# Optimization experiments

Hardware: AMD Instinct MI355X
Metric: run time of the kernel (lower is better)

## Reference

```python
import jax, jax.numpy as jnp
import numpy as np

SIGMA = 2048.0
N, D = 8192, 1024


def setup_inputs() -> dict:
    key = jax.random.key(0)
    kx, ky = jax.random.split(key)
    x = jax.random.normal(kx, (N, D), dtype=jnp.float32)
    y = jax.random.normal(ky, (N, D), dtype=jnp.float32)
    return {"x": x, "y": y}


def reference(x, y):
    x = x.astype(jnp.float32)
    y = y.astype(jnp.float32)
    # squared L2 norms, shape (N, 1)
    xn = jnp.sum(x * x, axis=1, keepdims=True)
    yn = jnp.sum(y * y, axis=1, keepdims=True)
    # Gram matrices (N, N)
    xx = x @ x.T
    xy = x @ y.T
    yy = y @ y.T
    first = jnp.mean(jnp.exp(-(xn + xn.T - 2.0 * xx) / SIGMA))
    second = jnp.mean(jnp.exp(-(yn + yn.T - 2.0 * yy) / SIGMA))
    third = jnp.mean(jnp.exp(-(xn + yn.T - 2.0 * xy) / SIGMA))
    return first + second - 2.0 * third
```

## Files before the change

kernel.cpp:

```cpp
#include <hip/hip_runtime.h>
#include <hip/hip_bf16.h>


#define N_ROWS 8192
#define DIM 1024
#define TWO_N 16384
#define BT 256
#define BK 64
#define NT2 64
#define NBLK2 (NT2 * (NT2 + 1) / 2)
#define GRID2 2048
#define NKT (DIM / BK)
#define QSCL (127.0f / 6.0f)
#define S2 ((6.0f / 127.0f) * (6.0f / 127.0f))
#define KFAC (-S2 / 2048.0f)

typedef int i32x4 __attribute__((ext_vector_type(4)));

typedef __attribute__((address_space(3))) unsigned int lds_u32_t;
typedef const __attribute__((address_space(1))) unsigned int glb_u32_t;

__device__ __forceinline__ void gload16(const void* g, void* l) {
    __builtin_amdgcn_global_load_lds((glb_u32_t*)g, (lds_u32_t*)l, 16, 0, 0);
}

#define SBAR() do { __builtin_amdgcn_sched_barrier(0); \
                    __builtin_amdgcn_s_barrier();      \
                    __builtin_amdgcn_sched_barrier(0); } while (0)
#define VMCNT(n) asm volatile("s_waitcnt vmcnt(" #n ")" ::: "memory")

__global__ __launch_bounds__(256) void mmd_convert_i8(const float* __restrict__ x,
                                                      const float* __restrict__ y,
                                                      int* __restrict__ zq,
                                                      int* __restrict__ zn) {
    int row = blockIdx.x * 4 + (threadIdx.x >> 6);
    int lane = threadIdx.x & 63;
    const float* p = (row < N_ROWS) ? (x + (size_t)row * DIM)
                                    : (y + (size_t)(row - N_ROWS) * DIM);
    int* q = zq + (size_t)row * (DIM / 4);
    int s = 0;
#pragma unroll
    for (int c = 0; c < 4; ++c) {
        int widx = lane + c * 64;
        float4 v = *(const float4*)(p + widx * 4);
        int q0 = (int)rintf(fminf(fmaxf(v.x * QSCL, -127.0f), 127.0f));
        int q1 = (int)rintf(fminf(fmaxf(v.y * QSCL, -127.0f), 127.0f));
        int q2 = (int)rintf(fminf(fmaxf(v.z * QSCL, -127.0f), 127.0f));
        int q3 = (int)rintf(fminf(fmaxf(v.w * QSCL, -127.0f), 127.0f));
        s += q0 * q0 + q1 * q1 + q2 * q2 + q3 * q3;
        q[widx] = (q0 & 0xff) | ((q1 & 0xff) << 8) | ((q2 & 0xff) << 16) | ((q3 & 0xff) << 24);
    }
#pragma unroll
    for (int o = 32; o > 0; o >>= 1) s += __shfl_down(s, o);
    if (lane == 0) zn[row] = s;
}

__global__ __launch_bounds__(512, 2) void mmd_main_i8(const char* __restrict__ zq,
                                                      const int* __restrict__ zn,
                                                      double* __restrict__ partials) {
    __shared__ __align__(16) char lsA[2][BT * BK];
    __shared__ __align__(16) char lsB[2][BT * BK];
    __shared__ double red[8];

    const int tid = threadIdx.x;
    const int bid0 = blockIdx.x;

    const int l = tid & 63;
    const int wid = tid >> 6;
    const int wr = wid >> 2;
    const int wc = wid & 3;
    const int fr = l & 15;
    const int fg = l >> 4;

    const int srow = tid >> 2;
    const int cswz = ((tid & 3) ^ ((tid >> 3) & 3)) * 16;
    char* lA = &lsA[0][0];
    char* lB = &lsB[0][0];
    const int t16 = tid * 16;

#define STG_A(buf, half, kt) \
    gload16(pA + (size_t)((half) * 128) * DIM + (kt) * BK, lA + (buf) * 16384 + (half) * 8192 + t16)
#define STG_B(buf, half, kt) \
    gload16(pB + (size_t)((half) * 128) * DIM + (kt) * BK, lB + (buf) * 16384 + (half) * 8192 + t16)
#define DS_A(buf, m) (*(const i32x4*)(lA + (buf) * 16384 + \
        (wr * 128 + (m) * 16 + fr) * 64 + ((fg ^ (((wr * 128 + (m) * 16 + fr) >> 1) & 3)) << 4)))
#define DS_B(buf, n) (*(const i32x4*)(lB + (buf) * 16384 + \
        (wc * 64 + (n) * 16 + fr) * 64 + ((fg ^ (((wc * 64 + (n) * 16 + fr) >> 1) & 3)) << 4)))

    const int npairs = (bid0 < NBLK2 - GRID2) ? 2 : 1;

#pragma unroll 1
    for (int pp = 0; pp < npairs; ++pp) {
        const int pid = pp ? (GRID2 + bid0) : bid0;
        const int bid = (pid & 7) * (NBLK2 / 8) + (pid >> 3);

        int tj = (int)((sqrtf(8.0f * (float)bid + 1.0f) - 1.0f) * 0.5f);
        while ((tj + 1) * (tj + 2) / 2 <= bid) ++tj;
        while (tj * (tj + 1) / 2 > bid) --tj;
        const int ti = bid - tj * (tj + 1) / 2;

        const int rA = ti * BT, rB = tj * BT;
        const float w = ((ti < 32) == (tj < 32)) ? 1.0f : -1.0f;
        const float factor = (ti == tj) ? w : 2.0f * w;

        const char* pA = zq + (size_t)(rA + srow) * DIM + cswz;
        const char* pB = zq + (size_t)(rB + srow) * DIM + cswz;

        i32x4 acc[8][4];
#pragma unroll
        for (int m = 0; m < 8; ++m)
#pragma unroll
            for (int n = 0; n < 4; ++n) acc[m][n] = (i32x4){0, 0, 0, 0};

        STG_A(0, 0, 0);
        STG_B(0, 0, 0);
        STG_B(0, 1, 0);
        STG_A(0, 1, 0);
        STG_A(1, 0, 1);
        VMCNT(1);
        SBAR();

        i32x4 a[4], b_cur[2], b_hi[2], b_nxt[2];
#pragma unroll
        for (int j = 0; j < 2; ++j) b_cur[j] = DS_B(0, j);

        for (int C = 0; C < NKT; ++C) {
            const int cb = C & 1, nb = cb ^ 1;

#pragma unroll
            for (int i = 0; i < 4; ++i) a[i] = DS_A(cb, i);
#pragma unroll
            for (int j = 0; j < 2; ++j) b_hi[j] = DS_B(cb, 2 + j);
            if (C < NKT - 1) STG_B(nb, 0, C + 1);
            SBAR();
            __builtin_amdgcn_s_setprio(1);
#pragma unroll
            for (int i = 0; i < 4; ++i)
#pragma unroll
                for (int j = 0; j < 2; ++j)
                    acc[i][j] = __builtin_amdgcn_mfma_i32_16x16x64_i8(a[i], b_cur[j], acc[i][j], 0, 0, 0);
            __builtin_amdgcn_s_setprio(0);
            SBAR();

            if (C < NKT - 1) STG_B(nb, 1, C + 1);
            SBAR();
            __builtin_amdgcn_s_setprio(1);
#pragma unroll
            for (int i = 0; i < 4; ++i)
#pragma unroll
                for (int j = 0; j < 2; ++j)
                    acc[i][2 + j] = __builtin_amdgcn_mfma_i32_16x16x64_i8(a[i], b_hi[j], acc[i][2 + j], 0, 0, 0);
            __builtin_amdgcn_s_setprio(0);
            SBAR();

#pragma unroll
            for (int i = 0; i < 4; ++i) a[i] = DS_A(cb, 4 + i);
            if (C < NKT - 1) {
                STG_A(nb, 1, C + 1);
                VMCNT(1);
            }
            SBAR();
            __builtin_amdgcn_s_setprio(1);
#pragma unroll
            for (int i = 0; i < 4; ++i)
#pragma unroll
                for (int j = 0; j < 2; ++j)
                    acc[4 + i][j] = __builtin_amdgcn_mfma_i32_16x16x64_i8(a[i], b_cur[j], acc[4 + i][j], 0, 0, 0);
            __builtin_amdgcn_s_setprio(0);
            SBAR();

            if (C < NKT - 1) {
#pragma unroll
                for (int j = 0; j < 2; ++j) b_nxt[j] = DS_B(nb, j);
                if (C < NKT - 2) {
                    STG_A(cb, 0, C + 2);
                    VMCNT(1);
                } else {
                    VMCNT(0);
                }
            }
            SBAR();
            __builtin_amdgcn_s_setprio(1);
#pragma unroll
            for (int i = 0; i < 4; ++i)
#pragma unroll
                for (int j = 0; j < 2; ++j)
                    acc[4 + i][2 + j] = __builtin_amdgcn_mfma_i32_16x16x64_i8(a[i], b_hi[j], acc[4 + i][2 + j], 0, 0, 0);
            __builtin_amdgcn_s_setprio(0);
            SBAR();

            if (C < NKT - 1) {
#pragma unroll
                for (int j = 0; j < 2; ++j) b_cur[j] = b_nxt[j];
            }
        }

        int rn[8][4];
#pragma unroll
        for (int m = 0; m < 8; ++m)
#pragma unroll
            for (int v = 0; v < 4; ++v)
                rn[m][v] = zn[rA + wr * 128 + m * 16 + fg * 4 + v];
        int cn[4];
#pragma unroll
        for (int n = 0; n < 4; ++n) cn[n] = zn[rB + wc * 64 + n * 16 + fr];

        float ls0 = 0.0f, ls1 = 0.0f;
#pragma unroll
        for (int m = 0; m < 8; ++m)
#pragma unroll
            for (int n = 0; n < 4; ++n)
#pragma unroll
                for (int v = 0; v < 4; ++v) {
                    int d2i = rn[m][v] + cn[n] - 2 * acc[m][n][v];
                    float e = __expf((float)d2i * KFAC);
                    if (v & 1) ls1 += e; else ls0 += e;
                }

        double d = (double)(ls0 + ls1);
#pragma unroll
        for (int o = 32; o > 0; o >>= 1) d += __shfl_down(d, o);
        if (l == 0) red[wid] = d;
        __syncthreads();
        if (tid == 0) {
            double t = 0.0;
#pragma unroll
            for (int i = 0; i < 8; ++i) t += red[i];
            partials[pid] = t * (double)factor;
        }
    }
#undef STG_A
#undef STG_B
#undef DS_A
#undef DS_B
}

__global__ __launch_bounds__(256) void mmd_reduce(const double* __restrict__ partials,
                                                  float* __restrict__ out, int n) {
    __shared__ double red[256];
    double s = 0.0;
    for (int i = threadIdx.x; i < n; i += 256) s += partials[i];
    red[threadIdx.x] = s;
    __syncthreads();
    for (int ofs = 128; ofs > 0; ofs >>= 1) {
        if (threadIdx.x < ofs) red[threadIdx.x] += red[threadIdx.x + ofs];
        __syncthreads();
    }
    if (threadIdx.x == 0)
        out[0] = (float)(red[0] / ((double)N_ROWS * (double)N_ROWS));
}

__global__ __launch_bounds__(256) void mmd_norms_f32(const float* __restrict__ x,
                                                     const float* __restrict__ y,
                                                     float* __restrict__ zn) {
    int row = blockIdx.x * 4 + (threadIdx.x >> 6);
    int lane = threadIdx.x & 63;
    const float* p = (row < N_ROWS) ? (x + (size_t)row * DIM)
                                    : (y + (size_t)(row - N_ROWS) * DIM);
    float s = 0.0f;
#pragma unroll
    for (int c = 0; c < 4; ++c) {
        float4 v = *(const float4*)(p + (size_t)(lane + c * 64) * 4);
        s = fmaf(v.x, v.x, s);
        s = fmaf(v.y, v.y, s);
        s = fmaf(v.z, v.z, s);
        s = fmaf(v.w, v.w, s);
    }
#pragma unroll
    for (int o = 32; o > 0; o >>= 1) s += __shfl_down(s, o);
    if (lane == 0) zn[row] = s;
}

__global__ __launch_bounds__(256) void mmd_main_f32(const float* __restrict__ x,
                                                    const float* __restrict__ y,
                                                    const float* __restrict__ zn,
                                                    double* __restrict__ partials) {
    int bid = blockIdx.x;
    int tj = (int)((sqrtf(8.0f * (float)bid + 1.0f) - 1.0f) * 0.5f);
    while ((tj + 1) * (tj + 2) / 2 <= bid) ++tj;
    while (tj * (tj + 1) / 2 > bid) --tj;
    int ti = bid - tj * (tj + 1) / 2;

    const float* A = (ti < 64) ? (x + (size_t)ti * 128 * DIM)
                               : (y + (size_t)(ti - 64) * 128 * DIM);
    const float* B = (tj < 64) ? (x + (size_t)tj * 128 * DIM)
                               : (y + (size_t)(tj - 64) * 128 * DIM);
    float w = ((ti < 64) == (tj < 64)) ? 1.0f : -1.0f;
    float factor = (ti == tj) ? w : 2.0f * w;

    __shared__ float fsa[32][128];
    __shared__ float fsb[32][128];
    __shared__ double red[256];

    int tid = threadIdx.x;
    int tx = tid & 15;
    int ty = tid >> 4;

    float acc[8][8];
#pragma unroll
    for (int r = 0; r < 8; ++r)
#pragma unroll
        for (int s = 0; s < 8; ++s) acc[r][s] = 0.0f;

    for (int k0 = 0; k0 < DIM; k0 += 32) {
#pragma unroll
        for (int u = 0; u < 4; ++u) {
            int f = tid + u * 256;
            int row = f >> 3;
            int kk = (f & 7) << 2;
            float4 va = *(const float4*)(A + (size_t)row * DIM + k0 + kk);
            float4 vb = *(const float4*)(B + (size_t)row * DIM + k0 + kk);
            fsa[kk + 0][row] = va.x; fsa[kk + 1][row] = va.y;
            fsa[kk + 2][row] = va.z; fsa[kk + 3][row] = va.w;
            fsb[kk + 0][row] = vb.x; fsb[kk + 1][row] = vb.y;
            fsb[kk + 2][row] = vb.z; fsb[kk + 3][row] = vb.w;
        }
        __syncthreads();
#pragma unroll 8
        for (int k = 0; k < 32; ++k) {
            float4 a0 = *(const float4*)&fsa[k][ty * 8];
            float4 a1 = *(const float4*)&fsa[k][ty * 8 + 4];
            float4 b0 = *(const float4*)&fsb[k][tx * 8];
            float4 b1 = *(const float4*)&fsb[k][tx * 8 + 4];
            float af[8] = {a0.x, a0.y, a0.z, a0.w, a1.x, a1.y, a1.z, a1.w};
            float bfv[8] = {b0.x, b0.y, b0.z, b0.w, b1.x, b1.y, b1.z, b1.w};
#pragma unroll
            for (int r = 0; r < 8; ++r)
#pragma unroll
                for (int s = 0; s < 8; ++s)
                    acc[r][s] = fmaf(af[r], bfv[s], acc[r][s]);
        }
        __syncthreads();
    }

    float xnrm[8], ynrm[8];
#pragma unroll
    for (int r = 0; r < 8; ++r) xnrm[r] = zn[ti * 128 + ty * 8 + r];
#pragma unroll
    for (int s = 0; s < 8; ++s) ynrm[s] = zn[tj * 128 + tx * 8 + s];

    float lsum = 0.0f;
#pragma unroll
    for (int r = 0; r < 8; ++r)
#pragma unroll
        for (int s = 0; s < 8; ++s) {
            float d2 = fmaf(-2.0f, acc[r][s], xnrm[r] + ynrm[s]);
            lsum += __expf(-d2 / 2048.0f);
        }

    red[tid] = (double)lsum;
    __syncthreads();
#pragma unroll
    for (int ofs = 128; ofs > 0; ofs >>= 1) {
        if (tid < ofs) red[tid] += red[tid + ofs];
        __syncthreads();
    }
    if (tid == 0) partials[bid] = red[0] * (double)factor;
}

extern "C" void kernel_launch(void* const* d_in, const int* in_sizes, int n_in,
                              void* d_out, int out_size, void* d_ws, size_t ws_size,
                              hipStream_t stream) {
    const float* x = (const float*)d_in[0];
    const float* y = (const float*)d_in[1];
    float* out = (float*)d_out;

    const size_t zq_bytes = (size_t)TWO_N * DIM;
    const size_t zn_bytes = (size_t)TWO_N * sizeof(int);
    const size_t pt_bytes = (size_t)NBLK2 * sizeof(double);
    const size_t need = zq_bytes + zn_bytes + pt_bytes;

    if (ws_size >= need) {
        int* zq = (int*)d_ws;
        int* zn = (int*)((char*)d_ws + zq_bytes);
        double* partials = (double*)((char*)d_ws + zq_bytes + zn_bytes);
        mmd_convert_i8<<<TWO_N / 4, 256, 0, stream>>>(x, y, zq, zn);
        mmd_main_i8<<<GRID2, 512, 0, stream>>>((const char*)zq, zn, partials);
        mmd_reduce<<<1, 256, 0, stream>>>(partials, out, NBLK2);
    } else {
        float* zn = (float*)d_ws;
        double* partials = (double*)((char*)d_ws + (size_t)TWO_N * sizeof(float));
        mmd_norms_f32<<<TWO_N / 4, 256, 0, stream>>>(x, y, zn);
        mmd_main_f32<<<128 * 129 / 2, 256, 0, stream>>>(x, y, zn, partials);
        mmd_reduce<<<1, 256, 0, stream>>>(partials, out, 128 * 129 / 2);
    }
}
```

Before: 211.3 us.

## Double K-tile depth to 128 bytes per stage in int8 MFMA pipeline

Doubles the K-tile from 64 to 128 int8 elements per pipeline stage. This halves the number of main-loop iterations and barriers and doubles the MFMA work between synchronisations. The LDS buffers grow to 64 KB per operand pair, the swizzle moves to an 8-way XOR, each staging macro issues two global-to-LDS loads, and the vmcnt thresholds change to match. A __syncthreads is added between tile pairs so the reduction array is not reused too early. The larger LDS footprint and register arrays may limit the two-blocks-per-CU occupancy.

```diff
diff --git a/kernel.cpp b/kernel.cpp
--- a/kernel.cpp
+++ b/kernel.cpp
@@ -6,11 +6,11 @@
 #define DIM 1024
 #define TWO_N 16384
 #define BT 256
-#define BK 64
+#define BKB 128
 #define NT2 64
 #define NBLK2 (NT2 * (NT2 + 1) / 2)
 #define GRID2 2048
-#define NKT (DIM / BK)
+#define NKT (DIM / BKB)
 #define QSCL (127.0f / 6.0f)
 #define S2 ((6.0f / 127.0f) * (6.0f / 127.0f))
 #define KFAC (-S2 / 2048.0f)
@@ -58,8 +58,8 @@
 __global__ __launch_bounds__(512, 2) void mmd_main_i8(const char* __restrict__ zq,
                                                       const int* __restrict__ zn,
                                                       double* __restrict__ partials) {
-    __shared__ __align__(16) char lsA[2][BT * BK];
-    __shared__ __align__(16) char lsB[2][BT * BK];
+    __shared__ __align__(16) char lsA[2][BT * BKB];
+    __shared__ __align__(16) char lsB[2][BT * BKB];
     __shared__ double red[8];
 
     const int tid = threadIdx.x;
@@ -72,20 +72,26 @@
     const int fr = l & 15;
     const int fg = l >> 4;
 
-    const int srow = tid >> 2;
-    const int cswz = ((tid & 3) ^ ((tid >> 3) & 3)) * 16;
+    const int srow = tid >> 3;
+    const int cswz = ((tid & 7) ^ ((tid >> 3) & 7)) * 16;
     char* lA = &lsA[0][0];
     char* lB = &lsB[0][0];
     const int t16 = tid * 16;
 
-#define STG_A(buf, half, kt) \
-    gload16(pA + (size_t)((half) * 128) * DIM + (kt) * BK, lA + (buf) * 16384 + (half) * 8192 + t16)
-#define STG_B(buf, half, kt) \
-    gload16(pB + (size_t)((half) * 128) * DIM + (kt) * BK, lB + (buf) * 16384 + (half) * 8192 + t16)
-#define DS_A(buf, m) (*(const i32x4*)(lA + (buf) * 16384 + \
-        (wr * 128 + (m) * 16 + fr) * 64 + ((fg ^ (((wr * 128 + (m) * 16 + fr) >> 1) & 3)) << 4)))
-#define DS_B(buf, n) (*(const i32x4*)(lB + (buf) * 16384 + \
-        (wc * 64 + (n) * 16 + fr) * 64 + ((fg ^ (((wc * 64 + (n) * 16 + fr) >> 1) & 3)) << 4)))
+#define STG_A(buf, half, kt) do {                                             \
+        const char* g_ = pA + (size_t)((half) * 128) * DIM + (kt) * BKB;      \
+        gload16(g_,            lA + (buf) * 32768 + (half) * 16384 + t16);        \
+        gload16(g_ + 64 * DIM, lA + (buf) * 32768 + (half) * 16384 + 8192 + t16); \
+    } while (0)
+#define STG_B(buf, half, kt) do {                                             \
+        const char* g_ = pB + (size_t)((half) * 128) * DIM + (kt) * BKB;      \
+        gload16(g_,            lB + (buf) * 32768 + (half) * 16384 + t16);        \
+        gload16(g_ + 64 * DIM, lB + (buf) * 32768 + (half) * 16384 + 8192 + t16); \
+    } while (0)
+#define DS_A(buf, m, s) (*(const i32x4*)(lA + (buf) * 32768 + \
+        (wr * 128 + (m) * 16 + fr) * BKB + ((((s) * 4 + fg) ^ (fr & 7)) << 4)))
+#define DS_B(buf, n, s) (*(const i32x4*)(lB + (buf) * 32768 + \
+        (wc * 64 + (n) * 16 + fr) * BKB + ((((s) * 4 + fg) ^ (fr & 7)) << 4)))
 
     const int npairs = (bid0 < NBLK2 - GRID2) ? 2 : 1;
 
@@ -117,64 +123,80 @@
         STG_B(0, 1, 0);
         STG_A(0, 1, 0);
         STG_A(1, 0, 1);
-        VMCNT(1);
+        VMCNT(2);
         SBAR();
 
-        i32x4 a[4], b_cur[2], b_hi[2], b_nxt[2];
-#pragma unroll
-        for (int j = 0; j < 2; ++j) b_cur[j] = DS_B(0, j);
+        i32x4 a[4][2], b_cur[2][2], b_hi[2][2], b_nxt[2][2];
+#pragma unroll
+        for (int j = 0; j < 2; ++j)
+#pragma unroll
+            for (int s = 0; s < 2; ++s) b_cur[j][s] = DS_B(0, j, s);
 
         for (int C = 0; C < NKT; ++C) {
             const int cb = C & 1, nb = cb ^ 1;
 
 #pragma unroll
-            for (int i = 0; i < 4; ++i) a[i] = DS_A(cb, i);
-#pragma unroll
-            for (int j = 0; j < 2; ++j) b_hi[j] = DS_B(cb, 2 + j);
+            for (int i = 0; i < 4; ++i)
+#pragma unroll
+                for (int s = 0; s < 2; ++s) a[i][s] = DS_A(cb, i, s);
             if (C < NKT - 1) STG_B(nb, 0, C + 1);
             SBAR();
             __builtin_amdgcn_s_setprio(1);
 #pragma unroll
+            for (int s = 0; s < 2; ++s)
+#pragma unroll
+                for (int i = 0; i < 4; ++i)
+#pragma unroll
+                    for (int j = 0; j < 2; ++j)
+                        acc[i][j] = __builtin_amdgcn_mfma_i32_16x16x64_i8(a[i][s], b_cur[j][s], acc[i][j], 0, 0, 0);
+            __builtin_amdgcn_s_setprio(0);
+            SBAR();
+
+#pragma unroll
+            for (int j = 0; j < 2; ++j)
+#pragma unroll
+                for (int s = 0; s < 2; ++s) b_hi[j][s] = DS_B(cb, 2 + j, s);
+            if (C < NKT - 1) STG_B(nb, 1, C + 1);
+            SBAR();
+            __builtin_amdgcn_s_setprio(1);
+#pragma unroll
+            for (int s = 0; s < 2; ++s)
+#pragma unroll
+                for (int i = 0; i < 4; ++i)
+#pragma unroll
+                    for (int j = 0; j < 2; ++j)
+                        acc[i][2 + j] = __builtin_amdgcn_mfma_i32_16x16x64_i8(a[i][s], b_hi[j][s], acc[i][2 + j], 0, 0, 0);
+            __builtin_amdgcn_s_setprio(0);
+            SBAR();
+
+#pragma unroll
             for (int i = 0; i < 4; ++i)
 #pragma unroll
-                for (int j = 0; j < 2; ++j)
-                    acc[i][j] = __builtin_amdgcn_mfma_i32_16x16x64_i8(a[i], b_cur[j], acc[i][j], 0, 0, 0);
-            __builtin_amdgcn_s_setprio(0);
-            SBAR();
-
-            if (C < NKT - 1) STG_B(nb, 1, C + 1);
-            SBAR();
-            __builtin_amdgcn_s_setprio(1);
-#pragma unroll
-            for (int i = 0; i < 4; ++i)
-#pragma unroll
-                for (int j = 0; j < 2; ++j)
-                    acc[i][2 + j] = __builtin_amdgcn_mfma_i32_16x16x64_i8(a[i], b_hi[j], acc[i][2 + j], 0, 0, 0);
-            __builtin_amdgcn_s_setprio(0);
-            SBAR();
-
-#pragma unroll
-            for (int i = 0; i < 4; ++i) a[i] = DS_A(cb, 4 + i);
+                for (int s = 0; s < 2; ++s) a[i][s] = DS_A(cb, 4 + i, s);
             if (C < NKT - 1) {
                 STG_A(nb, 1, C + 1);
-                VMCNT(1);
+                VMCNT(2);
             }
             SBAR();
             __builtin_amdgcn_s_setprio(1);
 #pragma unroll
-            for (int i = 0; i < 4; ++i)
+            for (int s = 0; s < 2; ++s)
+#pragma unroll
+                for (int i = 0; i < 4; ++i)
+#pragma unroll
+                    for (int j = 0; j < 2; ++j)
+                        acc[4 + i][j] = __builtin_amdgcn_mfma_i32_16x16x64_i8(a[i][s], b_cur[j][s], acc[4 + i][j], 0, 0, 0);
+            __builtin_amdgcn_s_setprio(0);
+            SBAR();
+
+            if (C < NKT - 1) {
 #pragma unroll
                 for (int j = 0; j < 2; ++j)
-                    acc[4 + i][j] = __builtin_amdgcn_mfma_i32_16x16x64_i8(a[i], b_cur[j], acc[4 + i][j], 0, 0, 0);
-            __builtin_amdgcn_s_setprio(0);
-            SBAR();
-
-            if (C < NKT - 1) {
-#pragma unroll
-                for (int j = 0; j < 2; ++j) b_nxt[j] = DS_B(nb, j);
+#pragma unroll
+                    for (int s = 0; s < 2; ++s) b_nxt[j][s] = DS_B(nb, j, s);
                 if (C < NKT - 2) {
                     STG_A(cb, 0, C + 2);
-                    VMCNT(1);
+                    VMCNT(2);
                 } else {
                     VMCNT(0);
                 }
@@ -182,16 +204,20 @@
             SBAR();
             __builtin_amdgcn_s_setprio(1);
 #pragma unroll
-            for (int i = 0; i < 4; ++i)
+            for (int s = 0; s < 2; ++s)
+#pragma unroll
+                for (int i = 0; i < 4; ++i)
+#pragma unroll
+                    for (int j = 0; j < 2; ++j)
+                        acc[4 + i][2 + j] = __builtin_amdgcn_mfma_i32_16x16x64_i8(a[i][s], b_hi[j][s], acc[4 + i][2 + j], 0, 0, 0);
+            __builtin_amdgcn_s_setprio(0);
+            SBAR();
+
+            if (C < NKT - 1) {
 #pragma unroll
                 for (int j = 0; j < 2; ++j)
-                    acc[4 + i][2 + j] = __builtin_amdgcn_mfma_i32_16x16x64_i8(a[i], b_hi[j], acc[4 + i][2 + j], 0, 0, 0);
-            __builtin_amdgcn_s_setprio(0);
-            SBAR();
-
-            if (C < NKT - 1) {
-#pragma unroll
-                for (int j = 0; j < 2; ++j) b_cur[j] = b_nxt[j];
+#pragma unroll
+                    for (int s = 0; s < 2; ++s) b_cur[j][s] = b_nxt[j][s];
             }
         }
 
@@ -228,6 +254,7 @@
             for (int i = 0; i < 8; ++i) t += red[i];
             partials[pid] = t * (double)factor;
         }
+        if (pp + 1 < npairs) __syncthreads();
     }
 #undef STG_A
 #undef STG_B
```

Result: faster. 203.4 us (-3.7%).
